# Optimization experiments

Hardware: AMD Instinct MI355X
Metric: run time of the kernel (lower is better)

## Reference

```python
import jax, jax.numpy as jnp
import numpy as np

N_BUS = 300
N_GBUS = 69
N_LINE = 411
G_BUS0 = 1
VMAX = 1.06
VMIN = 0.94
L_LIMIT = 1.0
LG_MAX = (1.0, 1.0, 1.0)
BATCH = 32768


def setup_inputs() -> dict:
    key = jax.random.key(0)
    ks = jax.random.split(key, 18)
    f = lambda k, s: jax.random.normal(k, s, dtype=jnp.float32)
    return {
        "Volt": f(ks[0], (BATCH, 2 * N_BUS)),
        "P_Gens": f(ks[1], (BATCH, 2 * N_GBUS)),
        "P_Loads": f(ks[2], (BATCH, 2 * N_BUS)),
        "n_o_l_p": f(ks[3], (BATCH, 2 * N_BUS)),
        "n_o_mu_g_u": f(ks[4], (BATCH, 2 * N_GBUS)),
        "n_o_mu_g_d": f(ks[5], (BATCH, 2 * N_GBUS)),
        "n_o_mu_v_u": f(ks[6], (BATCH, N_BUS)),
        "n_o_mu_v_d": f(ks[7], (BATCH, N_BUS)),
        "n_o_mu_i_u": f(ks[8], (BATCH, N_LINE)),
        "Y": f(ks[9], (2 * N_BUS, 2 * N_BUS)) * 0.1,
        "Yconj": f(ks[10], (2 * N_BUS, 2 * N_BUS)) * 0.1,
        "Ybr": f(ks[11], (2 * N_LINE, 2 * N_LINE)) * 0.1,
        "IM": f(ks[12], (2 * N_LINE, 2 * N_BUS)) * 0.1,
        "Map_g": f(ks[13], (2 * N_GBUS, 2 * N_BUS)) * 0.1,
        "Map_L": f(ks[14], (2 * N_BUS, 2 * N_BUS)) * 0.1,
        "Gen_max": jax.random.uniform(ks[15], (1, 2 * N_GBUS), dtype=jnp.float32) + 0.5,
        "Gen_min": -jax.random.uniform(ks[16], (1, 2 * N_GBUS), dtype=jnp.float32) - 0.5,
        "C_Pg": f(ks[17], (1, N_GBUS)),
    }


def reference(Volt, P_Gens, P_Loads, n_o_l_p, n_o_mu_g_u, n_o_mu_g_d,
              n_o_mu_v_u, n_o_mu_v_d, n_o_mu_i_u,
              Y, Yconj, Ybr, IM, Map_g, Map_L, Gen_max, Gen_min, C_Pg):
    n = N_BUS
    B = Volt.shape[0]
    Bf = jnp.asarray(B, Volt.dtype)
    relu = jax.nn.relu

    Vre = Volt[:, :n]
    Vim = Volt[:, n:2 * n]

    # --- per-bus quadratic-form loop, vectorized ---------------------------
    # diag(Volt @ (M_i Y) @ Volt^T)[b] = Volt[b,i-1]*(Y[i-1]@Volt[b]) + Volt[b,n+i-1]*(Y[n+i-1]@Volt[b])
    quad_p = Volt * (Volt @ Y.T)      # [B, 2n]; quad_p[b,r] = Volt[b,r]*(Y[r]@Volt[b])
    quad_q = Volt * (Volt @ Yconj.T)  # [B, 2n]
    # TF broadcast quirk: [B] diag + [B,1] mismatch -> [B,B], reduce_sum(axis=1)
    # gives sum_j diag[j] (scalar) + B * mismatch[b].  Loop runs i = 1..n-1.
    scalar_pq = (jnp.sum(quad_p[:, 0:n - 1]) + jnp.sum(quad_p[:, n:2 * n - 1])
                 + jnp.sum(quad_q[:, 0:n - 1]) + jnp.sum(quad_q[:, n:2 * n - 1]))
    mism = P_Loads @ Map_L - P_Gens @ Map_g  # [B, 2n]
    mism_sum = jnp.sum(mism[:, 0:n - 1], axis=1) + jnp.sum(mism[:, n:2 * n - 1], axis=1)

    kkt = jnp.sum(jnp.abs(Volt[:, n + G_BUS0 - 1]))  # scalar seed
    kkt = kkt + scalar_pq + Bf * mism_sum            # -> [B]

    # --- inequality / complementarity terms --------------------------------
    kkt = kkt + jnp.sum(relu(P_Gens - Gen_max), axis=1)
    kkt = kkt + jnp.sum(relu(Gen_min - P_Gens), axis=1)

    v_up = Vre ** 2 + Vim ** 2 - VMAX ** 2
    v_dn = VMIN ** 2 - Vre ** 2 + Vim ** 2  # sign kept exactly as in original
    kkt = kkt + jnp.sum(relu(v_up), axis=1)
    kkt = kkt + jnp.sum(relu(v_dn), axis=1)

    Ibr = Volt @ IM.T @ Ybr.T  # == (Ybr @ (IM @ Volt^T))^T, [B, 2*n_line]
    i_up = Ibr[:, :N_LINE] ** 2 + Ibr[:, N_LINE:] ** 2 - L_LIMIT ** 2
    kkt = kkt + jnp.sum(relu(i_up), axis=1)

    kkt = kkt + jnp.sum(jnp.abs(n_o_mu_g_u * (P_Gens - Gen_max)), axis=1) / N_GBUS
    kkt = kkt + jnp.sum(jnp.abs(n_o_mu_g_d * (Gen_min - P_Gens)), axis=1) / N_GBUS
    kkt = kkt + jnp.sum(jnp.abs(n_o_mu_v_u * v_up), axis=1)
    kkt = kkt + jnp.sum(jnp.abs(n_o_mu_v_d * v_dn), axis=1)
    kkt = kkt + jnp.sum(jnp.abs(n_o_mu_i_u * i_up), axis=1)

    # --- stationarity w.r.t. generator injections ---------------------------
    C_Qg = jnp.zeros((1, N_GBUS), Volt.dtype)
    cost = jnp.concatenate([C_Pg, C_Qg], axis=1)  # [1, 2*n_gbus]
    stat = (n_o_mu_g_u * LG_MAX[1] - n_o_mu_g_d * LG_MAX[2]
            + (n_o_l_p * LG_MAX[0]) @ Map_g.T - cost)
    kkt = kkt + jnp.sum(jnp.abs(stat), axis=1)

    # --- dual feasibility ----------------------------------------------------
    kkt = kkt + jnp.sum(relu(-n_o_mu_g_u), axis=1)
    kkt = kkt + jnp.sum(relu(-n_o_mu_g_d), axis=1)
    kkt = kkt + jnp.sum(relu(-n_o_mu_v_u), axis=1)
    kkt = kkt + jnp.sum(relu(-n_o_mu_v_d), axis=1)
    kkt = kkt + jnp.sum(relu(-n_o_mu_i_u), axis=1)
    return kkt
```

## Files before the change

kernel.cpp:

```cpp
#include <hip/hip_runtime.h>

#define BATCH   32768
#define NLINE   411
#define NTILES  14
#define RTILES  256

typedef __attribute__((ext_vector_type(8))) short  short8;
typedef __attribute__((ext_vector_type(4))) float  f32x4;

#define WS_SCALAR   0
#define WS_KROWS    64
#define WS_MAPL     131136
#define WS_MAPG     133536
#define WS_ATMP     134144
#define WS_BMF      2106944
#define WS_VBF      4400704
#define WS_NEED_FAST (4400704 + 41943040)
#define WS_ZERO_BYTES 2106944

__device__ __forceinline__ unsigned short f2bf(float f) {
    unsigned int u = __float_as_uint(f);
    unsigned int r = (u + 0x7FFFu + ((u >> 16) & 1u)) >> 16;
    return (unsigned short)r;
}

#if defined(__has_builtin)
#  if __has_builtin(__builtin_amdgcn_cvt_pk_bf16_f32)
#    define HAVE_PK_BF16 1
#  endif
#endif

__device__ __forceinline__ unsigned int pk2bf(float a, float b) {
#ifdef HAVE_PK_BF16
    typedef __bf16 bf16x2 __attribute__((ext_vector_type(2)));
    bf16x2 r = __builtin_amdgcn_cvt_pk_bf16_f32(a, b);
    return __builtin_bit_cast(unsigned int, r);
#else
    return (unsigned int)f2bf(a) | ((unsigned int)f2bf(b) << 16);
#endif
}

__global__ __launch_bounds__(256) void prep_A(const float* __restrict__ Ybr,
                                              const float* __restrict__ IM,
                                              float* __restrict__ Atmp) {
    int bid = blockIdx.x;
    int ks = bid & 3;
    int t2 = bid >> 2;
    int bc = t2 % 10, br = t2 / 10;
    int r0 = br * 64, c0 = bc * 64;
    int kb = ks * 206;
    int ke = (kb + 206 < 822) ? kb + 206 : 822;

    __shared__ float Yt[64][33];
    __shared__ float Xt[32][65];
    int t = threadIdx.x;
    int tx = t & 15, ty = t >> 4;
    float c[4][4] = {};

    for (int kk = kb; kk < ke; kk += 32) {
        __syncthreads();
        for (int e = t; e < 2048; e += 256) {
            int yr = e >> 5, yk = e & 31;
            int gr = r0 + yr, gk = kk + yk;
            Yt[yr][yk] = (gr < 822 && gk < ke) ? Ybr[(size_t)gr * 822 + gk] : 0.f;
        }
        for (int e = t; e < 2048; e += 256) {
            int xk = e >> 6, xc = e & 63;
            int gk = kk + xk, gc = c0 + xc;
            Xt[xk][xc] = (gk < ke && gc < 600) ? IM[(size_t)gk * 600 + gc] : 0.f;
        }
        __syncthreads();
        for (int k2 = 0; k2 < 32; ++k2) {
            float a[4], b[4];
#pragma unroll
            for (int ii = 0; ii < 4; ++ii) a[ii] = Yt[ty * 4 + ii][k2];
#pragma unroll
            for (int jj = 0; jj < 4; ++jj) b[jj] = Xt[k2][tx * 4 + jj];
#pragma unroll
            for (int ii = 0; ii < 4; ++ii)
#pragma unroll
                for (int jj = 0; jj < 4; ++jj) c[ii][jj] += a[ii] * b[jj];
        }
    }
#pragma unroll
    for (int ii = 0; ii < 4; ++ii)
#pragma unroll
        for (int jj = 0; jj < 4; ++jj) {
            int gr = r0 + ty * 4 + ii, gc = c0 + tx * 4 + jj;
            if (gr < 822 && gc < 600) atomicAdd(Atmp + (size_t)gr * 600 + gc, c[ii][jj]);
        }
}

__global__ __launch_bounds__(256) void prep_misc(
    const float* __restrict__ MapL, const float* __restrict__ Mapg,
    float* __restrict__ mapL_s, float* __restrict__ mapg_s,
    const float* __restrict__ Y, const float* __restrict__ Yconj,
    const float* __restrict__ Atmp, unsigned short* __restrict__ BmF,
    const float* __restrict__ Volt, unsigned short* __restrict__ Vbf, int doConv) {
    int bid = blockIdx.x;
    int t = threadIdx.x;
    int w = t >> 6, lane = t & 63;

    if (bid < 185) {
        int row = bid * 4 + w;
        const float* src;
        float* dst;
        if (row < 600)      { src = MapL + (size_t)row * 600; dst = mapL_s + row; }
        else if (row < 738) { src = Mapg + (size_t)(row - 600) * 600; dst = mapg_s + (row - 600); }
        else return;
        float s = 0.f;
        for (int j = lane; j < 600; j += 64)
            if (j != 299 && j != 599) s += src[j];
        for (int m = 32; m >= 1; m >>= 1) s += __shfl_xor(s, m);
        if (lane == 0) *dst = s;
    } else if (bid < 745) {
        int b2 = bid - 185;
        int ntkc = b2 >> 2;
        int nt = ntkc / 10, kc = ntkc % 10;
        int S = (b2 & 3) * 256 + t;
        int ig = S >> 7, ks = (S >> 6) & 1, ln = S & 63;
        int rc = ig * 16 + (ln & 15);
        int kb = ks * 32 + ((ln >> 4) << 3);
        int n = nt * 128 + rc;
        unsigned short out[8];
#pragma unroll
        for (int j = 0; j < 8; ++j) {
            int k = kc * 64 + kb + j;
            float v = 0.f;
            if (k < 600) {
                if (n < 600) {
                    if (n != 299 && n != 599)
                        v = Y[(size_t)n * 600 + k] + Yconj[(size_t)n * 600 + k];
                } else if (n >= 640 && n < 1536) {
                    int idx = n - 640;
                    int l = idx >> 1, h = idx & 1;
                    if (l < NLINE) v = Atmp[(size_t)(h * NLINE + l) * 600 + k];
                } else if (n >= 1536) {
                    int g = n - 1536;
                    if (g < 138) v = Mapg[(size_t)g * 600 + k];
                }
            }
            out[j] = f2bf(v);
        }
        *(short8*)(BmF + (size_t)(ntkc * 1024 + S) * 8) = *(short8*)out;
    } else {
        if (!doConv) return;
        int b = (bid - 745) * 4 + w;
        for (int c = lane * 4; c < 600; c += 256) {
            f32x4 x = *(const f32x4*)(Volt + (size_t)b * 600 + c);
            uint2 p;
            p.x = pk2bf(x[0], x[1]);
            p.y = pk2bf(x[2], x[3]);
            *(uint2*)(Vbf + (size_t)b * 640 + c) = p;
        }
        if (lane < 10) {
            uint2 z = make_uint2(0u, 0u);
            *(uint2*)(Vbf + (size_t)b * 640 + 600 + lane * 4) = z;
        }
    }
}

__global__ __launch_bounds__(256, 2) void kkt_main(
    const float* __restrict__ Volt, const float* __restrict__ nolp,
    const float* __restrict__ PG, const float* __restrict__ PL,
    const float* __restrict__ mu_gu, const float* __restrict__ mu_gd,
    const float* __restrict__ mu_vu, const float* __restrict__ mu_vd,
    const float* __restrict__ mu_iu,
    const float* __restrict__ Gmax, const float* __restrict__ Gmin,
    const float* __restrict__ CPg,
    const unsigned short* __restrict__ Vbf, const unsigned short* __restrict__ BmF,
    const float* __restrict__ mapLs, const float* __restrict__ mapgs,
    float* __restrict__ kkt_rows, float* __restrict__ scalar_acc, int useVbf) {

    int idx = blockIdx.x;
    int xcd = idx & 7;
    int q = idx >> 3;
    int nt = q % NTILES;
    int rg = q / NTILES;
    int rt = rg * 8 + xcd;
    int b0 = rt * 128;

    int t = threadIdx.x;
    int lane = t & 63, w = t >> 6, wr = w >> 1, wc = w & 1;

    __shared__ short8 Asm[2][1024];
    __shared__ short8 Bsm[2][1024];
    __shared__ float  mls[600];
    __shared__ float  redbuf[4];

    bool fastA = (nt < 12) && useVbf;
    const float* Af32 = (nt < 12) ? Volt : nolp;

    for (int j = t; j < 600; j += 256) mls[j] = mapLs[j];

    int rcA[4], kbA[4];
#pragma unroll
    for (int m = 0; m < 4; ++m) {
        int S = m * 256 + t;
        int ig = S >> 7, ks = (S >> 6) & 1, ln = S & 63;
        rcA[m] = ig * 16 + (ln & 15);
        kbA[m] = ks * 32 + ((ln >> 4) << 3);
    }

    auto issueB = [&](int kc, int pb) {
        const unsigned short* bSrc = BmF + (size_t)(nt * 10 + kc) * 8192;
#pragma unroll
        for (int m = 0; m < 4; ++m) {
            int S = m * 256 + t;
            __builtin_amdgcn_global_load_lds(
                (const __attribute__((address_space(1))) unsigned int*)(bSrc + (size_t)S * 8),
                (__attribute__((address_space(3))) unsigned int*)&Bsm[pb][S], 16, 0, 0);
        }
    };
    auto issueA = [&](int kc, int pb) {
#pragma unroll
        for (int m = 0; m < 4; ++m) {
            int S = m * 256 + t;
            __builtin_amdgcn_global_load_lds(
                (const __attribute__((address_space(1))) unsigned int*)(Vbf + (size_t)(b0 + rcA[m]) * 640 + kc * 64 + kbA[m]),
                (__attribute__((address_space(3))) unsigned int*)&Asm[pb][S], 16, 0, 0);
        }
    };
    auto loadA = [&](int kc, f32x4* xa) {
#pragma unroll
        for (int m = 0; m < 4; ++m) {
            int gk = kc * 64 + kbA[m];
            if (gk < 600) {
                const f32x4* p = (const f32x4*)(Af32 + (size_t)(b0 + rcA[m]) * 600 + gk);
                xa[2 * m] = p[0]; xa[2 * m + 1] = p[1];
            } else {
                f32x4 z = {0.f, 0.f, 0.f, 0.f};
                xa[2 * m] = z; xa[2 * m + 1] = z;
            }
        }
    };
    auto writeA = [&](const f32x4* xa, int pb) {
#pragma unroll
        for (int m = 0; m < 4; ++m) {
            int S = m * 256 + t;
            f32x4 a = xa[2 * m], b = xa[2 * m + 1];
            Asm[pb][S] = __builtin_bit_cast(short8,
                make_uint4(pk2bf(a[0], a[1]), pk2bf(a[2], a[3]),
                           pk2bf(b[0], b[1]), pk2bf(b[2], b[3])));
        }
    };

    issueB(0, 0);
    if (fastA) issueA(0, 0);
    else { f32x4 x0[8]; loadA(0, x0); writeA(x0, 0); }
    __syncthreads();

    f32x4 acc[4][4] = {};
    float dscal = 0.f;
    int cur = 0;

    for (int kc = 0; kc < 10; ++kc) {
        int nxt = cur ^ 1;
        bool havN = (kc < 9);
        f32x4 xa[8];
        if (havN) {
            issueB(kc + 1, nxt);
            if (fastA) issueA(kc + 1, nxt);
            else       loadA(kc + 1, xa);
        }

        const short8* Ak = Asm[cur];
        const short8* Bk = Bsm[cur];
#pragma unroll
        for (int ks = 0; ks < 2; ++ks) {
            short8 af[4], bfr[4];
#pragma unroll
            for (int ii = 0; ii < 4; ++ii) af[ii] = Ak[((wr * 4 + ii) * 2 + ks) * 64 + lane];
#pragma unroll
            for (int jj = 0; jj < 4; ++jj) bfr[jj] = Bk[((wc * 4 + jj) * 2 + ks) * 64 + lane];
#pragma unroll
            for (int ii = 0; ii < 4; ++ii)
#pragma unroll
                for (int jj = 0; jj < 4; ++jj)
                    acc[ii][jj] = __builtin_amdgcn_mfma_f32_16x16x32_bf16(af[ii], bfr[jj], acc[ii][jj], 0, 0, 0);
        }

        if (kc < 3) {
            int i = kc * 4 + w;
            int rl = nt + 14 * i;
            if (i < 10 && rl < 128) {
                int r = b0 + rl;
                const float* vrow = Volt + (size_t)r * 600;
                float sd = 0.f;
                for (int j = lane * 4; j < 300; j += 256) {
                    f32x4 vr  = *(const f32x4*)(vrow + j);
                    f32x4 vi  = *(const f32x4*)(vrow + 300 + j);
                    f32x4 muu = *(const f32x4*)(mu_vu + (size_t)r * 300 + j);
                    f32x4 mud = *(const f32x4*)(mu_vd + (size_t)r * 300 + j);
#pragma unroll
                    for (int e = 0; e < 4; ++e) {
                        float sq = vr[e] * vr[e], si = vi[e] * vi[e];
                        float vu = sq + si - 1.1236f;
                        float vd = 0.8836f - sq + si;
                        sd += fmaxf(vu, 0.f) + fmaxf(vd, 0.f)
                            + fabsf(muu[e] * vu) + fabsf(mud[e] * vd)
                            + fmaxf(-muu[e], 0.f) + fmaxf(-mud[e], 0.f);
                    }
                }
                float s2 = 0.f;
                for (int j = lane * 4; j < 600; j += 256) {
                    f32x4 pl = *(const f32x4*)(PL + (size_t)r * 600 + j);
#pragma unroll
                    for (int e = 0; e < 4; ++e) s2 += pl[e] * mls[j + e];
                }
                sd += 32768.0f * s2;
                for (int m = 32; m >= 1; m >>= 1) sd += __shfl_xor(sd, m);
                if (lane == 0) {
                    atomicAdd(kkt_rows + r, sd);
                    dscal += fabsf(vrow[300]);
                }
            }
        }

        if (havN && !fastA) writeA(xa, nxt);

        __syncthreads();
        cur = nxt;
    }

    if (lane == 0 && dscal != 0.f) atomicAdd(scalar_acc, dscal);

    if (nt < 5) {
        float qa = 0.f;
#pragma unroll
        for (int ii = 0; ii < 4; ++ii)
#pragma unroll
            for (int jj = 0; jj < 4; ++jj)
#pragma unroll
                for (int r2 = 0; r2 < 4; ++r2) {
                    int row = wr * 64 + ii * 16 + ((lane >> 4) << 2) + r2;
                    int col = nt * 128 + wc * 64 + jj * 16 + (lane & 15);
                    if (col < 600) {
                        float v = Volt[(size_t)(b0 + row) * 600 + col];
                        qa += acc[ii][jj][r2] * v;
                    }
                }
        for (int m = 32; m >= 1; m >>= 1) qa += __shfl_xor(qa, m);
        if (lane == 0) redbuf[w] = qa;
        __syncthreads();
        if (t == 0) atomicAdd(scalar_acc, redbuf[0] + redbuf[1] + redbuf[2] + redbuf[3]);
    } else if (nt < 12) {
        float racc[16];
#pragma unroll
        for (int s = 0; s < 16; ++s) racc[s] = 0.f;
#pragma unroll
        for (int ii = 0; ii < 4; ++ii)
#pragma unroll
            for (int jj = 0; jj < 4; ++jj)
#pragma unroll
                for (int r2 = 0; r2 < 4; ++r2) {
                    float u = acc[ii][jj][r2];
                    float up = __shfl_xor(u, 1);
                    int col = nt * 128 + wc * 64 + jj * 16 + (lane & 15);
                    int l = (col - 640) >> 1;
                    float contrib = 0.f;
                    if (l < NLINE && !(lane & 1)) {
                        int row = wr * 64 + ii * 16 + ((lane >> 4) << 2) + r2;
                        float iu = u * u + up * up - 1.0f;
                        float mu = mu_iu[(size_t)(b0 + row) * NLINE + l];
                        contrib = fmaxf(iu, 0.f) + fabsf(mu * iu) + fmaxf(-mu, 0.f);
                    }
                    racc[ii * 4 + r2] += contrib;
                }
#pragma unroll
        for (int s = 0; s < 16; ++s) {
            float v = racc[s];
            v += __shfl_xor(v, 1); v += __shfl_xor(v, 2);
            v += __shfl_xor(v, 4); v += __shfl_xor(v, 8);
            if ((lane & 15) == 0) {
                int row = wr * 64 + (s >> 2) * 16 + ((lane >> 4) << 2) + (s & 3);
                atomicAdd(kkt_rows + b0 + row, v);
            }
        }
    } else {
        float racc[16];
#pragma unroll
        for (int s = 0; s < 16; ++s) racc[s] = 0.f;
#pragma unroll
        for (int ii = 0; ii < 4; ++ii)
#pragma unroll
            for (int jj = 0; jj < 4; ++jj)
#pragma unroll
                for (int r2 = 0; r2 < 4; ++r2) {
                    int col = nt * 128 + wc * 64 + jj * 16 + (lane & 15);
                    int g = col - 1536;
                    float contrib = 0.f;
                    if (g < 138) {
                        int row = wr * 64 + ii * 16 + ((lane >> 4) << 2) + r2;
                        size_t ix = (size_t)(b0 + row) * 138 + g;
                        float u = acc[ii][jj][r2];
                        float gu = mu_gu[ix], gd = mu_gd[ix], pg = PG[ix];
                        float gmx = Gmax[g], gmn = Gmin[g];
                        float cst = (g < 69) ? CPg[g] : 0.f;
                        float t1 = pg - gmx, t2 = gmn - pg;
                        float st = u + gu - gd - cst;
                        contrib = fabsf(st) + fmaxf(t1, 0.f) + fmaxf(t2, 0.f)
                                + (fabsf(gu * t1) + fabsf(gd * t2)) * (1.0f / 69.0f)
                                + fmaxf(-gu, 0.f) + fmaxf(-gd, 0.f)
                                - 32768.0f * pg * mapgs[g];
                    }
                    racc[ii * 4 + r2] += contrib;
                }
#pragma unroll
        for (int s = 0; s < 16; ++s) {
            float v = racc[s];
            v += __shfl_xor(v, 1); v += __shfl_xor(v, 2);
            v += __shfl_xor(v, 4); v += __shfl_xor(v, 8);
            if ((lane & 15) == 0) {
                int row = wr * 64 + (s >> 2) * 16 + ((lane >> 4) << 2) + (s & 3);
                atomicAdd(kkt_rows + b0 + row, v);
            }
        }
    }
}

__global__ void finalize_k(const float* __restrict__ kkt_rows, const float* __restrict__ scalar_acc,
                           float* __restrict__ out) {
    int i = blockIdx.x * 256 + threadIdx.x;
    out[i] = kkt_rows[i] + scalar_acc[0];
}

extern "C" void kernel_launch(void* const* d_in, const int* in_sizes, int n_in,
                              void* d_out, int out_size, void* d_ws, size_t ws_size,
                              hipStream_t stream) {
    const float* Volt  = (const float*)d_in[0];
    const float* PG    = (const float*)d_in[1];
    const float* PL    = (const float*)d_in[2];
    const float* nolp  = (const float*)d_in[3];
    const float* mu_gu = (const float*)d_in[4];
    const float* mu_gd = (const float*)d_in[5];
    const float* mu_vu = (const float*)d_in[6];
    const float* mu_vd = (const float*)d_in[7];
    const float* mu_iu = (const float*)d_in[8];
    const float* Y     = (const float*)d_in[9];
    const float* Yconj = (const float*)d_in[10];
    const float* Ybr   = (const float*)d_in[11];
    const float* IM    = (const float*)d_in[12];
    const float* Mapg  = (const float*)d_in[13];
    const float* MapL  = (const float*)d_in[14];
    const float* Gmax  = (const float*)d_in[15];
    const float* Gmin  = (const float*)d_in[16];
    const float* CPg   = (const float*)d_in[17];

    char* ws = (char*)d_ws;
    float* scalar_acc       = (float*)(ws + WS_SCALAR);
    float* kkt_rows         = (float*)(ws + WS_KROWS);
    float* mapLs            = (float*)(ws + WS_MAPL);
    float* mapgs            = (float*)(ws + WS_MAPG);
    float* Atmp             = (float*)(ws + WS_ATMP);
    unsigned short* BmF     = (unsigned short*)(ws + WS_BMF);
    unsigned short* Vbf     = (unsigned short*)(ws + WS_VBF);

    int useVbf = (ws_size >= (size_t)WS_NEED_FAST) ? 1 : 0;

    hipMemsetAsync(d_ws, 0, WS_ZERO_BYTES, stream);
    prep_A<<<520, 256, 0, stream>>>(Ybr, IM, Atmp);
    prep_misc<<<185 + 560 + 8192, 256, 0, stream>>>(MapL, Mapg, mapLs, mapgs,
                                                    Y, Yconj, Atmp, BmF, Volt, Vbf, useVbf);
    kkt_main<<<RTILES * NTILES, 256, 0, stream>>>(Volt, nolp, PG, PL, mu_gu, mu_gd,
                                                  mu_vu, mu_vd, mu_iu, Gmax, Gmin, CPg,
                                                  Vbf, BmF, mapLs, mapgs,
                                                  kkt_rows, scalar_acc, useVbf);
    finalize_k<<<BATCH / 256, 256, 0, stream>>>(kkt_rows, scalar_acc, (float*)d_out);
}
```

Before: 816.7 us.

## Pre-swizzle Volt into MFMA fragment layout and single-buffer LDS for occupancy

The conversion pass now writes bf16 Volt already laid out in the per-tile, per-k-chunk fragment order the GEMM consumes. This lets the main kernel stream contiguous 16KB chunks into LDS the same way it loads B. The main kernel drops LDS double buffering and register prefetch so it fits four workgroups per CU instead of two, relying on occupancy rather than in-block pipelining to hide load latency. The cost is an extra barrier per k-chunk and no overlap of loads with MFMA inside a block.

```diff
diff --git a/kernel.cpp b/kernel.cpp
--- a/kernel.cpp
+++ b/kernel.cpp
@@ -96,7 +96,7 @@
     float* __restrict__ mapL_s, float* __restrict__ mapg_s,
     const float* __restrict__ Y, const float* __restrict__ Yconj,
     const float* __restrict__ Atmp, unsigned short* __restrict__ BmF,
-    const float* __restrict__ Volt, unsigned short* __restrict__ Vbf, int doConv) {
+    const float* __restrict__ Volt, unsigned short* __restrict__ VbfF, int doConv) {
     int bid = blockIdx.x;
     int t = threadIdx.x;
     int w = t >> 6, lane = t & 63;
@@ -145,22 +145,31 @@
         *(short8*)(BmF + (size_t)(ntkc * 1024 + S) * 8) = *(short8*)out;
     } else {
         if (!doConv) return;
-        int b = (bid - 745) * 4 + w;
-        for (int c = lane * 4; c < 600; c += 256) {
-            f32x4 x = *(const f32x4*)(Volt + (size_t)b * 600 + c);
-            uint2 p;
-            p.x = pk2bf(x[0], x[1]);
-            p.y = pk2bf(x[2], x[3]);
-            *(uint2*)(Vbf + (size_t)b * 640 + c) = p;
-        }
-        if (lane < 10) {
-            uint2 z = make_uint2(0u, 0u);
-            *(uint2*)(Vbf + (size_t)b * 640 + 600 + lane * 4) = z;
+        int b2 = bid - 745;
+        int rt = b2 / 10, kc = b2 % 10;
+        int b0 = rt * 128;
+        unsigned short* dst = VbfF + (size_t)(rt * 10 + kc) * 8192;
+#pragma unroll
+        for (int m = 0; m < 4; ++m) {
+            int S = m * 256 + t;
+            int ig = S >> 7, ks = (S >> 6) & 1, ln = S & 63;
+            int rc = ig * 16 + (ln & 15);
+            int kb = ks * 32 + ((ln >> 4) << 3);
+            int k = kc * 64 + kb;
+            short8 outv = (short8)0;
+            if (k < 600) {
+                const f32x4* p = (const f32x4*)(Volt + (size_t)(b0 + rc) * 600 + k);
+                f32x4 a = p[0], b = p[1];
+                outv = __builtin_bit_cast(short8,
+                    make_uint4(pk2bf(a[0], a[1]), pk2bf(a[2], a[3]),
+                               pk2bf(b[0], b[1]), pk2bf(b[2], b[3])));
+            }
+            *(short8*)(dst + (size_t)S * 8) = outv;
         }
     }
 }
 
-__global__ __launch_bounds__(256, 2) void kkt_main(
+__global__ __launch_bounds__(256, 4) void kkt_main(
     const float* __restrict__ Volt, const float* __restrict__ nolp,
     const float* __restrict__ PG, const float* __restrict__ PL,
     const float* __restrict__ mu_gu, const float* __restrict__ mu_gd,
@@ -168,7 +177,7 @@
     const float* __restrict__ mu_iu,
     const float* __restrict__ Gmax, const float* __restrict__ Gmin,
     const float* __restrict__ CPg,
-    const unsigned short* __restrict__ Vbf, const unsigned short* __restrict__ BmF,
+    const unsigned short* __restrict__ VbfF, const unsigned short* __restrict__ BmF,
     const float* __restrict__ mapLs, const float* __restrict__ mapgs,
     float* __restrict__ kkt_rows, float* __restrict__ scalar_acc, int useVbf) {
 
@@ -183,8 +192,8 @@
     int t = threadIdx.x;
     int lane = t & 63, w = t >> 6, wr = w >> 1, wc = w & 1;
 
-    __shared__ short8 Asm[2][1024];
-    __shared__ short8 Bsm[2][1024];
+    __shared__ short8 Asm[1024];
+    __shared__ short8 Bsm[1024];
     __shared__ float  mls[600];
     __shared__ float  redbuf[4];
 
@@ -192,6 +201,7 @@
     const float* Af32 = (nt < 12) ? Volt : nolp;
 
     for (int j = t; j < 600; j += 256) mls[j] = mapLs[j];
+    __syncthreads();
 
     int rcA[4], kbA[4];
 #pragma unroll
@@ -202,82 +212,52 @@
         kbA[m] = ks * 32 + ((ln >> 4) << 3);
     }
 
-    auto issueB = [&](int kc, int pb) {
-        const unsigned short* bSrc = BmF + (size_t)(nt * 10 + kc) * 8192;
-#pragma unroll
-        for (int m = 0; m < 4; ++m) {
-            int S = m * 256 + t;
-            __builtin_amdgcn_global_load_lds(
-                (const __attribute__((address_space(1))) unsigned int*)(bSrc + (size_t)S * 8),
-                (__attribute__((address_space(3))) unsigned int*)&Bsm[pb][S], 16, 0, 0);
-        }
-    };
-    auto issueA = [&](int kc, int pb) {
-#pragma unroll
-        for (int m = 0; m < 4; ++m) {
-            int S = m * 256 + t;
-            __builtin_amdgcn_global_load_lds(
-                (const __attribute__((address_space(1))) unsigned int*)(Vbf + (size_t)(b0 + rcA[m]) * 640 + kc * 64 + kbA[m]),
-                (__attribute__((address_space(3))) unsigned int*)&Asm[pb][S], 16, 0, 0);
-        }
-    };
-    auto loadA = [&](int kc, f32x4* xa) {
-#pragma unroll
-        for (int m = 0; m < 4; ++m) {
-            int gk = kc * 64 + kbA[m];
-            if (gk < 600) {
-                const f32x4* p = (const f32x4*)(Af32 + (size_t)(b0 + rcA[m]) * 600 + gk);
-                xa[2 * m] = p[0]; xa[2 * m + 1] = p[1];
-            } else {
-                f32x4 z = {0.f, 0.f, 0.f, 0.f};
-                xa[2 * m] = z; xa[2 * m + 1] = z;
-            }
-        }
-    };
-    auto writeA = [&](const f32x4* xa, int pb) {
-#pragma unroll
-        for (int m = 0; m < 4; ++m) {
-            int S = m * 256 + t;
-            f32x4 a = xa[2 * m], b = xa[2 * m + 1];
-            Asm[pb][S] = __builtin_bit_cast(short8,
-                make_uint4(pk2bf(a[0], a[1]), pk2bf(a[2], a[3]),
-                           pk2bf(b[0], b[1]), pk2bf(b[2], b[3])));
-        }
-    };
-
-    issueB(0, 0);
-    if (fastA) issueA(0, 0);
-    else { f32x4 x0[8]; loadA(0, x0); writeA(x0, 0); }
-    __syncthreads();
-
     f32x4 acc[4][4] = {};
     float dscal = 0.f;
-    int cur = 0;
 
     for (int kc = 0; kc < 10; ++kc) {
-        int nxt = cur ^ 1;
-        bool havN = (kc < 9);
-        f32x4 xa[8];
-        if (havN) {
-            issueB(kc + 1, nxt);
-            if (fastA) issueA(kc + 1, nxt);
-            else       loadA(kc + 1, xa);
-        }
-
-        const short8* Ak = Asm[cur];
-        const short8* Bk = Bsm[cur];
-#pragma unroll
-        for (int ks = 0; ks < 2; ++ks) {
-            short8 af[4], bfr[4];
-#pragma unroll
-            for (int ii = 0; ii < 4; ++ii) af[ii] = Ak[((wr * 4 + ii) * 2 + ks) * 64 + lane];
-#pragma unroll
-            for (int jj = 0; jj < 4; ++jj) bfr[jj] = Bk[((wc * 4 + jj) * 2 + ks) * 64 + lane];
-#pragma unroll
-            for (int ii = 0; ii < 4; ++ii)
-#pragma unroll
-                for (int jj = 0; jj < 4; ++jj)
-                    acc[ii][jj] = __builtin_amdgcn_mfma_f32_16x16x32_bf16(af[ii], bfr[jj], acc[ii][jj], 0, 0, 0);
+        if (kc) __syncthreads();
+
+        {
+            const unsigned short* bSrc = BmF + (size_t)(nt * 10 + kc) * 8192;
+#pragma unroll
+            for (int m = 0; m < 4; ++m) {
+                int S = m * 256 + t;
+                __builtin_amdgcn_global_load_lds(
+                    (const __attribute__((address_space(1))) unsigned int*)(bSrc + (size_t)S * 8),
+                    (__attribute__((address_space(3))) unsigned int*)&Bsm[S], 16, 0, 0);
+            }
+        }
+        if (fastA) {
+            const unsigned short* aSrc = VbfF + (size_t)(rt * 10 + kc) * 8192;
+#pragma unroll
+            for (int m = 0; m < 4; ++m) {
+                int S = m * 256 + t;
+                __builtin_amdgcn_global_load_lds(
+                    (const __attribute__((address_space(1))) unsigned int*)(aSrc + (size_t)S * 8),
+                    (__attribute__((address_space(3))) unsigned int*)&Asm[S], 16, 0, 0);
+            }
+        } else {
+            f32x4 xa[8];
+#pragma unroll
+            for (int m = 0; m < 4; ++m) {
+                int gk = kc * 64 + kbA[m];
+                if (gk < 600) {
+                    const f32x4* p = (const f32x4*)(Af32 + (size_t)(b0 + rcA[m]) * 600 + gk);
+                    xa[2 * m] = p[0]; xa[2 * m + 1] = p[1];
+                } else {
+                    f32x4 z = {0.f, 0.f, 0.f, 0.f};
+                    xa[2 * m] = z; xa[2 * m + 1] = z;
+                }
+            }
+#pragma unroll
+            for (int m = 0; m < 4; ++m) {
+                int S = m * 256 + t;
+                f32x4 a = xa[2 * m], b = xa[2 * m + 1];
+                Asm[S] = __builtin_bit_cast(short8,
+                    make_uint4(pk2bf(a[0], a[1]), pk2bf(a[2], a[3]),
+                               pk2bf(b[0], b[1]), pk2bf(b[2], b[3])));
+            }
         }
 
         if (kc < 3) {
@@ -317,10 +297,21 @@
             }
         }
 
-        if (havN && !fastA) writeA(xa, nxt);
-
         __syncthreads();
-        cur = nxt;
+
+#pragma unroll
+        for (int ks = 0; ks < 2; ++ks) {
+            short8 af[4], bfr[4];
+#pragma unroll
+            for (int ii = 0; ii < 4; ++ii) af[ii] = Asm[((wr * 4 + ii) * 2 + ks) * 64 + lane];
+#pragma unroll
+            for (int jj = 0; jj < 4; ++jj) bfr[jj] = Bsm[((wc * 4 + jj) * 2 + ks) * 64 + lane];
+#pragma unroll
+            for (int ii = 0; ii < 4; ++ii)
+#pragma unroll
+                for (int jj = 0; jj < 4; ++jj)
+                    acc[ii][jj] = __builtin_amdgcn_mfma_f32_16x16x32_bf16(af[ii], bfr[jj], acc[ii][jj], 0, 0, 0);
+        }
     }
 
     if (lane == 0 && dscal != 0.f) atomicAdd(scalar_acc, dscal);
@@ -454,17 +445,17 @@
     float* mapgs            = (float*)(ws + WS_MAPG);
     float* Atmp             = (float*)(ws + WS_ATMP);
     unsigned short* BmF     = (unsigned short*)(ws + WS_BMF);
-    unsigned short* Vbf     = (unsigned short*)(ws + WS_VBF);
+    unsigned short* VbfF    = (unsigned short*)(ws + WS_VBF);
 
     int useVbf = (ws_size >= (size_t)WS_NEED_FAST) ? 1 : 0;
 
     hipMemsetAsync(d_ws, 0, WS_ZERO_BYTES, stream);
     prep_A<<<520, 256, 0, stream>>>(Ybr, IM, Atmp);
-    prep_misc<<<185 + 560 + 8192, 256, 0, stream>>>(MapL, Mapg, mapLs, mapgs,
-                                                    Y, Yconj, Atmp, BmF, Volt, Vbf, useVbf);
+    prep_misc<<<185 + 560 + 2560, 256, 0, stream>>>(MapL, Mapg, mapLs, mapgs,
+                                                    Y, Yconj, Atmp, BmF, Volt, VbfF, useVbf);
     kkt_main<<<RTILES * NTILES, 256, 0, stream>>>(Volt, nolp, PG, PL, mu_gu, mu_gd,
                                                   mu_vu, mu_vd, mu_iu, Gmax, Gmin, CPg,
-                                                  Vbf, BmF, mapLs, mapgs,
+                                                  VbfF, BmF, mapLs, mapgs,
                                                   kkt_rows, scalar_acc, useVbf);
     finalize_k<<<BATCH / 256, 256, 0, stream>>>(kkt_rows, scalar_acc, (float*)d_out);
 }
```

Result: faster. 747.2 us (-8.5%).
